# Optimization experiments

Measured on AMD Instinct MI355X. Metric: run time of the kernel, lower is better.

Reference implementation:

```python
import jax, jax.numpy as jnp
import numpy as np

NUM_GENES = 4384
D_MODEL = 128


def setup_inputs() -> dict:
    key = jax.random.key(0)
    ks = jax.random.split(key, 8)
    B = 8
    return {
        "mutation_input": jax.random.normal(ks[0], (B, NUM_GENES, 4), dtype=jnp.float32),
        "external_V": jax.random.normal(ks[1], (NUM_GENES, D_MODEL), dtype=jnp.float32),
        "W_in": jax.random.normal(ks[2], (4, D_MODEL), dtype=jnp.float32) * 0.5,
        "b_in": jnp.zeros((D_MODEL,), dtype=jnp.float32),
        "key_param": jax.random.normal(ks[3], (NUM_GENES, D_MODEL), dtype=jnp.float32),
        "W1": jax.random.normal(ks[4], (D_MODEL, 64), dtype=jnp.float32) * (1.0 / np.sqrt(D_MODEL)),
        "b1": jnp.zeros((64,), dtype=jnp.float32),
        "W2": jax.random.normal(ks[5], (64, 26), dtype=jnp.float32) * 0.125,
        "b2": jnp.zeros((26,), dtype=jnp.float32),
    }


def reference(mutation_input, external_V, W_in, b_in, key_param, W1, b1, W2, b2):
    # Q: [B, G, D]
    Q = jnp.einsum("bgf,fd->bgd", mutation_input, W_in) + b_in
    scale = 1.0 / jnp.sqrt(jnp.asarray(Q.shape[-1], Q.dtype))
    # scores: [B, G, G] -- full matrix as in the original module
    scores = jnp.einsum("bqd,kd->bqk", Q, key_param) * scale
    attn = jax.nn.softmax(scores, axis=-1)
    # attention output: [B, G, D]
    attn_out = jnp.einsum("bqk,kd->bqd", attn, external_V)
    mean_out = attn_out.mean(axis=1)  # [B, D]
    h = jax.nn.gelu(mean_out @ W1 + b1, approximate=False)
    out = h @ W2 + b2  # [B, 26]
    return out
```

## Files before the change

kernel.cpp:

```cpp
#include <hip/hip_runtime.h>
#include <hip/hip_bf16.h>

#define NUM_GENES 4384
#define GPAD 4480
#define DM 128
#define ROWB 256
#define LDS_STRIDE 272
#define NTILES 137
#define NCHUNK 4
#define TILES_PER_CHUNK 35

typedef __attribute__((ext_vector_type(8))) short short8;
typedef __attribute__((ext_vector_type(16))) float floatx16;

__global__ void zero_lw(float* l, float* w, float* meanbuf) {
    int i = blockIdx.x * 256 + threadIdx.x;
    l[i] = 0.f;
    w[i] = 0.f;
    if (i < 1024) meanbuf[i] = 0.f;
}

__global__ void prep_q(const float* __restrict__ mut, const float* __restrict__ W_in,
                       const float* __restrict__ b_in, __hip_bfloat16* __restrict__ Qb) {
    int idx = blockIdx.x * 256 + threadIdx.x;
    int d = idx & 127;
    int g = (idx >> 7) % GPAD;
    int b = idx / (GPAD * 128);
    float v = 0.f;
    if (g < NUM_GENES) {
        const float* m = mut + ((size_t)b * NUM_GENES + g) * 4;
        v = b_in[d] + m[0] * W_in[d] + m[1] * W_in[128 + d]
                    + m[2] * W_in[256 + d] + m[3] * W_in[384 + d];
        v *= 0.088388347648318447f;
    }
    Qb[idx] = __float2bfloat16(v);
}

__global__ void prep_k(const float* __restrict__ key, __hip_bfloat16* __restrict__ Kb) {
    int idx = blockIdx.x * 256 + threadIdx.x;
    int g = idx >> 7;
    float v = (g < NUM_GENES) ? key[idx] : 0.f;
    Kb[idx] = __float2bfloat16(v);
}

__global__ void recip_k(float* l) {
    int i = blockIdx.x * 256 + threadIdx.x;
    l[i] = 1.0f / l[i];
}

template <bool PB>
__global__ __launch_bounds__(256)
void phase_kernel(const __hip_bfloat16* __restrict__ Qb,
                  const __hip_bfloat16* __restrict__ Kb,
                  const float* __restrict__ linv,
                  float* __restrict__ out) {
    __shared__ __align__(16) char tile[32 * LDS_STRIDE];

    int rb    = blockIdx.x;
    int chunk = blockIdx.y;
    int b     = blockIdx.z;

    const char* resident = (const char*)(PB ? Kb : (Qb + (size_t)b * GPAD * DM));
    const char* stream   = (const char*)(PB ? (Qb + (size_t)b * GPAD * DM) : Kb);

    int t = threadIdx.x;
    int lane = t & 63, wid = t >> 6;
    int m = lane & 31, half = lane >> 5;

    short8 afrag[8];
    const char* arow = resident + (size_t)(rb * 128 + wid * 32 + m) * ROWB;
#pragma unroll
    for (int dsl = 0; dsl < 8; ++dsl)
        afrag[dsl] = *(const short8*)(arow + dsl * 32 + half * 16);

    float lacc[16];
#pragma unroll
    for (int r = 0; r < 16; ++r) lacc[r] = 0.f;

    int t0 = chunk * TILES_PER_CHUNK;
    int t1 = min(NTILES, t0 + TILES_PER_CHUNK);
    int sr = t >> 3, sc = t & 7;

    for (int kt = t0; kt < t1; ++kt) {
        const char* src = stream + (size_t)(kt * 32 + sr) * ROWB + sc * 32;
        float4 v0 = *(const float4*)src;
        float4 v1 = *(const float4*)(src + 16);
        __syncthreads();
        char* dst = tile + sr * LDS_STRIDE + sc * 32;
        *(float4*)dst = v0;
        *(float4*)(dst + 16) = v1;
        __syncthreads();

        floatx16 acc;
#pragma unroll
        for (int r = 0; r < 16; ++r) acc[r] = 0.f;
#pragma unroll
        for (int dsl = 0; dsl < 8; ++dsl) {
            short8 bfrag = *(const short8*)(tile + m * LDS_STRIDE + dsl * 32 + half * 16);
            acc = __builtin_amdgcn_mfma_f32_32x32x16_bf16(afrag[dsl], bfrag, acc, 0, 0, 0);
        }

        float scl = 1.0f;
        if (PB) scl = linv[b * GPAD + kt * 32 + m];
#pragma unroll
        for (int r = 0; r < 16; ++r)
            lacc[r] += __expf(acc[r]) * scl;
    }

#pragma unroll
    for (int off = 1; off <= 16; off <<= 1) {
#pragma unroll
        for (int r = 0; r < 16; ++r)
            lacc[r] += __shfl_xor(lacc[r], off, 64);
    }

    if (m == 0) {
        float* ob = out + b * GPAD + rb * 128 + wid * 32 + 4 * half;
#pragma unroll
        for (int r = 0; r < 16; ++r) {
            int row = (r & 3) + 8 * (r >> 2);
            atomicAdd(ob + row, lacc[r]);
        }
    }
}

__global__ __launch_bounds__(256)
void mean_k(const float* __restrict__ w, const float* __restrict__ V,
            float* __restrict__ meanbuf) {
    int rb = blockIdx.x, b = blockIdx.y;
    int t = threadIdx.x;
    int d = t & 127, half = t >> 7;
    int g0 = rb * 128 + half * 64;
    int nv = NUM_GENES - g0;
    if (nv > 64) nv = 64;
    float a = 0.f;
    if (nv > 0) {
        const float* wb = w + b * GPAD + g0;
        const float* Vp = V + (size_t)g0 * 128 + d;
        for (int k = 0; k < nv; ++k)
            a += wb[k] * Vp[(size_t)k * 128];
    }
    atomicAdd(meanbuf + b * 128 + d, a);
}

__global__ void mlp_k(const float* __restrict__ meanbuf,
                      const float* __restrict__ W1, const float* __restrict__ b1,
                      const float* __restrict__ W2, const float* __restrict__ b2,
                      float* __restrict__ out) {
    int b = blockIdx.x, t = threadIdx.x;
    __shared__ float sh[64];
    const float* mb = meanbuf + b * 128;
    float s = b1[t];
    for (int d = 0; d < 128; ++d)
        s += (mb[d] * (1.0f / 4384.0f)) * W1[d * 64 + t];
    sh[t] = 0.5f * s * (1.0f + erff(s * 0.70710678118654752f));
    __syncthreads();
    if (t < 26) {
        float o = b2[t];
        for (int j = 0; j < 64; ++j) o += sh[j] * W2[j * 26 + t];
        out[b * 26 + t] = o;
    }
}

extern "C" void kernel_launch(void* const* d_in, const int* in_sizes, int n_in,
                              void* d_out, int out_size, void* d_ws, size_t ws_size,
                              hipStream_t stream) {
    const float* mut  = (const float*)d_in[0];
    const float* V    = (const float*)d_in[1];
    const float* W_in = (const float*)d_in[2];
    const float* b_in = (const float*)d_in[3];
    const float* key  = (const float*)d_in[4];
    const float* W1   = (const float*)d_in[5];
    const float* b1   = (const float*)d_in[6];
    const float* W2   = (const float*)d_in[7];
    const float* b2   = (const float*)d_in[8];
    float* out = (float*)d_out;

    char* ws = (char*)d_ws;
    __hip_bfloat16* Qb = (__hip_bfloat16*)(ws);
    __hip_bfloat16* Kb = (__hip_bfloat16*)(ws + 9175040);
    float* lbuf        = (float*)(ws + 10321920);
    float* wbuf        = (float*)(ws + 10465280);
    float* meanbuf     = (float*)(ws + 10608640);

    zero_lw<<<140, 256, 0, stream>>>(lbuf, wbuf, meanbuf);
    prep_q<<<17920, 256, 0, stream>>>(mut, W_in, b_in, Qb);
    prep_k<<<2240, 256, 0, stream>>>(key, Kb);

    dim3 grid(35, NCHUNK, 8);
    phase_kernel<false><<<grid, 256, 0, stream>>>(Qb, Kb, lbuf, lbuf);
    recip_k<<<140, 256, 0, stream>>>(lbuf);
    phase_kernel<true><<<grid, 256, 0, stream>>>(Qb, Kb, lbuf, wbuf);

    mean_k<<<dim3(35, 8), 256, 0, stream>>>(wbuf, V, meanbuf);
    mlp_k<<<8, 64, 0, stream>>>(meanbuf, W1, b1, W2, b2, out);
}
```

Before: 246.5 us.

## Double resident rows per wave, prefetch next stream tile, use exp2 with folded log2e

Each wave now holds two 32-row A fragments, so every LDS B fragment feeds two MFMAs, and blocks cover 256 resident rows. GPAD grows to 4608 and the chunk split changes to 6 chunks of 23 tiles. The next stream tile is loaded into registers while the current one is being computed. The softmax exponent becomes a hardware exp2, with log2(e) folded into the Q scale. The cost is more register pressure and more padded rows whose work is wasted.

Result: faster. 227.0 us (-7.9%).

```diff
diff --git a/kernel.cpp b/kernel.cpp
--- a/kernel.cpp
+++ b/kernel.cpp
@@ -2,16 +2,26 @@
 #include <hip/hip_bf16.h>
 
 #define NUM_GENES 4384
-#define GPAD 4480
+#define GPAD 4608
 #define DM 128
 #define ROWB 256
 #define LDS_STRIDE 272
 #define NTILES 137
-#define NCHUNK 4
-#define TILES_PER_CHUNK 35
+#define RB_BLOCKS 18
+#define NCHUNK 6
+#define TPC 23
 
 typedef __attribute__((ext_vector_type(8))) short short8;
 typedef __attribute__((ext_vector_type(16))) float floatx16;
+
+#if defined(__has_builtin)
+#  if __has_builtin(__builtin_amdgcn_exp2f)
+#    define FAST_EXP2(x) __builtin_amdgcn_exp2f(x)
+#  endif
+#endif
+#ifndef FAST_EXP2
+#  define FAST_EXP2(x) exp2f(x)
+#endif
 
 __global__ void zero_lw(float* l, float* w, float* meanbuf) {
     int i = blockIdx.x * 256 + threadIdx.x;
@@ -31,7 +41,7 @@
         const float* m = mut + ((size_t)b * NUM_GENES + g) * 4;
         v = b_in[d] + m[0] * W_in[d] + m[1] * W_in[128 + d]
                     + m[2] * W_in[256 + d] + m[3] * W_in[384 + d];
-        v *= 0.088388347648318447f;
+        v *= (0.08838834764831845f * 1.4426950408889634f);
     }
     Qb[idx] = __float2bfloat16(v);
 }
@@ -67,59 +77,83 @@
     int lane = t & 63, wid = t >> 6;
     int m = lane & 31, half = lane >> 5;
 
-    short8 afrag[8];
-    const char* arow = resident + (size_t)(rb * 128 + wid * 32 + m) * ROWB;
-#pragma unroll
-    for (int dsl = 0; dsl < 8; ++dsl)
-        afrag[dsl] = *(const short8*)(arow + dsl * 32 + half * 16);
-
-    float lacc[16];
-#pragma unroll
-    for (int r = 0; r < 16; ++r) lacc[r] = 0.f;
-
-    int t0 = chunk * TILES_PER_CHUNK;
-    int t1 = min(NTILES, t0 + TILES_PER_CHUNK);
+    short8 afrag[2][8];
+#pragma unroll
+    for (int g = 0; g < 2; ++g) {
+        const char* arow = resident + (size_t)(rb * 256 + wid * 64 + g * 32 + m) * ROWB;
+#pragma unroll
+        for (int dsl = 0; dsl < 8; ++dsl)
+            afrag[g][dsl] = *(const short8*)(arow + dsl * 32 + half * 16);
+    }
+
+    float lacc[2][16];
+#pragma unroll
+    for (int g = 0; g < 2; ++g)
+#pragma unroll
+        for (int r = 0; r < 16; ++r) lacc[g][r] = 0.f;
+
+    int t0 = chunk * TPC;
+    int t1 = min(NTILES, t0 + TPC);
     int sr = t >> 3, sc = t & 7;
+    char* dst = tile + sr * LDS_STRIDE + sc * 32;
+
+    const char* src = stream + (size_t)(t0 * 32 + sr) * ROWB + sc * 32;
+    float4 v0 = *(const float4*)src;
+    float4 v1 = *(const float4*)(src + 16);
 
     for (int kt = t0; kt < t1; ++kt) {
-        const char* src = stream + (size_t)(kt * 32 + sr) * ROWB + sc * 32;
-        float4 v0 = *(const float4*)src;
-        float4 v1 = *(const float4*)(src + 16);
         __syncthreads();
-        char* dst = tile + sr * LDS_STRIDE + sc * 32;
         *(float4*)dst = v0;
         *(float4*)(dst + 16) = v1;
         __syncthreads();
 
-        floatx16 acc;
-#pragma unroll
-        for (int r = 0; r < 16; ++r) acc[r] = 0.f;
+        if (kt + 1 < t1) {
+            const char* s2 = stream + (size_t)((kt + 1) * 32 + sr) * ROWB + sc * 32;
+            v0 = *(const float4*)s2;
+            v1 = *(const float4*)(s2 + 16);
+        }
+
+        floatx16 acc0, acc1;
+#pragma unroll
+        for (int r = 0; r < 16; ++r) { acc0[r] = 0.f; acc1[r] = 0.f; }
 #pragma unroll
         for (int dsl = 0; dsl < 8; ++dsl) {
             short8 bfrag = *(const short8*)(tile + m * LDS_STRIDE + dsl * 32 + half * 16);
-            acc = __builtin_amdgcn_mfma_f32_32x32x16_bf16(afrag[dsl], bfrag, acc, 0, 0, 0);
-        }
-
-        float scl = 1.0f;
-        if (PB) scl = linv[b * GPAD + kt * 32 + m];
-#pragma unroll
-        for (int r = 0; r < 16; ++r)
-            lacc[r] += __expf(acc[r]) * scl;
-    }
-
-#pragma unroll
-    for (int off = 1; off <= 16; off <<= 1) {
-#pragma unroll
-        for (int r = 0; r < 16; ++r)
-            lacc[r] += __shfl_xor(lacc[r], off, 64);
-    }
+            acc0 = __builtin_amdgcn_mfma_f32_32x32x16_bf16(afrag[0][dsl], bfrag, acc0, 0, 0, 0);
+            acc1 = __builtin_amdgcn_mfma_f32_32x32x16_bf16(afrag[1][dsl], bfrag, acc1, 0, 0, 0);
+        }
+
+        if (PB) {
+            float scl = linv[b * GPAD + kt * 32 + m];
+#pragma unroll
+            for (int r = 0; r < 16; ++r) {
+                lacc[0][r] = fmaf(FAST_EXP2(acc0[r]), scl, lacc[0][r]);
+                lacc[1][r] = fmaf(FAST_EXP2(acc1[r]), scl, lacc[1][r]);
+            }
+        } else {
+#pragma unroll
+            for (int r = 0; r < 16; ++r) {
+                lacc[0][r] += FAST_EXP2(acc0[r]);
+                lacc[1][r] += FAST_EXP2(acc1[r]);
+            }
+        }
+    }
+
+#pragma unroll
+    for (int off = 1; off <= 16; off <<= 1)
+#pragma unroll
+        for (int g = 0; g < 2; ++g)
+#pragma unroll
+            for (int r = 0; r < 16; ++r)
+                lacc[g][r] += __shfl_xor(lacc[g][r], off, 64);
 
     if (m == 0) {
-        float* ob = out + b * GPAD + rb * 128 + wid * 32 + 4 * half;
-#pragma unroll
-        for (int r = 0; r < 16; ++r) {
-            int row = (r & 3) + 8 * (r >> 2);
-            atomicAdd(ob + row, lacc[r]);
+#pragma unroll
+        for (int g = 0; g < 2; ++g) {
+            float* ob = out + b * GPAD + rb * 256 + wid * 64 + g * 32 + 4 * half;
+#pragma unroll
+            for (int r = 0; r < 16; ++r)
+                atomicAdd(ob + (r & 3) + 8 * (r >> 2), lacc[g][r]);
         }
     }
 }
@@ -178,18 +212,18 @@
 
     char* ws = (char*)d_ws;
     __hip_bfloat16* Qb = (__hip_bfloat16*)(ws);
-    __hip_bfloat16* Kb = (__hip_bfloat16*)(ws + 9175040);
-    float* lbuf        = (float*)(ws + 10321920);
-    float* wbuf        = (float*)(ws + 10465280);
-    float* meanbuf     = (float*)(ws + 10608640);
-
-    zero_lw<<<140, 256, 0, stream>>>(lbuf, wbuf, meanbuf);
-    prep_q<<<17920, 256, 0, stream>>>(mut, W_in, b_in, Qb);
-    prep_k<<<2240, 256, 0, stream>>>(key, Kb);
-
-    dim3 grid(35, NCHUNK, 8);
+    __hip_bfloat16* Kb = (__hip_bfloat16*)(ws + 9437184);
+    float* lbuf        = (float*)(ws + 10616832);
+    float* wbuf        = (float*)(ws + 10764288);
+    float* meanbuf     = (float*)(ws + 10911744);
+
+    zero_lw<<<144, 256, 0, stream>>>(lbuf, wbuf, meanbuf);
+    prep_q<<<18432, 256, 0, stream>>>(mut, W_in, b_in, Qb);
+    prep_k<<<2304, 256, 0, stream>>>(key, Kb);
+
+    dim3 grid(RB_BLOCKS, NCHUNK, 8);
     phase_kernel<false><<<grid, 256, 0, stream>>>(Qb, Kb, lbuf, lbuf);
-    recip_k<<<140, 256, 0, stream>>>(lbuf);
+    recip_k<<<144, 256, 0, stream>>>(lbuf);
     phase_kernel<true><<<grid, 256, 0, stream>>>(Qb, Kb, lbuf, wbuf);
 
     mean_k<<<dim3(35, 8), 256, 0, stream>>>(wbuf, V, meanbuf);
```
